# Performance work log

Measured on AMD Instinct MI355X. Metric: run time of the kernel, lower is better.

The kernel has to match this reference:

```python
import jax, jax.numpy as jnp
import numpy as np

B, S, D, DK = 8192, 3, 2048, 1024  # S fixed to 3 by Linear(3,3)/Bilinear(3,3,3)
NORM_FACT = 1.0 / np.sqrt(DK)


def setup_inputs() -> dict:
    key = jax.random.key(0)
    ks = jax.random.split(key, 9)
    s_lin = 1.0 / np.sqrt(D)
    s3 = 1.0 / np.sqrt(3.0)
    return {
        "img": jax.random.normal(ks[0], (B, S, D), jnp.float32),
        "text": jax.random.normal(ks[1], (B, S, D), jnp.float32),
        "Wq": jax.random.uniform(ks[2], (DK, D), jnp.float32, -s_lin, s_lin),
        "bq": jax.random.uniform(ks[3], (DK,), jnp.float32, -s_lin, s_lin),
        "Wk": jax.random.uniform(ks[4], (DK, D), jnp.float32, -s_lin, s_lin),
        "bk": jax.random.uniform(ks[5], (DK,), jnp.float32, -s_lin, s_lin),
        "Wj": jax.random.uniform(ks[6], (3, 3), jnp.float32, -s3, s3),
        "bj": jax.random.uniform(ks[7], (3,), jnp.float32, -s3, s3),
        "Wbil": jax.random.uniform(ks[8], (3, 3, 3), jnp.float32, -s3, s3),
    }


def reference(img, text, Wq, bq, Wk, bk, Wj, bj, Wbil):
    # Projections: [B, S, DK]
    Q_i = jnp.einsum("bsd,kd->bsk", img, Wq) + bq
    K_i = jnp.einsum("bsd,kd->bsk", img, Wk) + bk
    Q_t = jnp.einsum("bsd,kd->bsk", text, Wq) + bq
    K_t = jnp.einsum("bsd,kd->bsk", text, Wk) + bk

    # [B, S, S] attention maps; note: scale applied AFTER softmax (faithful to source)
    atten_it = jax.nn.softmax(jnp.einsum("bqk,bsk->bqs", Q_i, K_t), axis=-1) * NORM_FACT
    atten_ii = jax.nn.softmax(jnp.einsum("bqk,bsk->bqs", Q_i, K_i), axis=-1) * NORM_FACT
    atten_tt = jax.nn.softmax(jnp.einsum("bqk,bsk->bqs", Q_t, K_t), axis=-1) * NORM_FACT

    def j_lin(x):  # Linear(3,3) on last dim
        return jnp.einsum("bqs,os->bqo", x, Wj) + bj

    def bilinear(x1, x2):  # Bilinear(3,3,3, bias=False)
        return jnp.einsum("bqi,oij,bqj->bqo", x1, Wbil, x2)

    j_it = j_lin(atten_it)
    atten_i = bilinear(j_it, j_lin(atten_ii))
    atten_t = bilinear(j_it, j_lin(atten_tt))

    output_i = jnp.einsum("bqs,bsd->bqd", atten_i, img)
    output_t = jnp.einsum("bqs,bsd->bqd", atten_t, text)
    return (output_i, output_t)
```

## Files before the change

### kernel.cpp

```cpp
#include <hip/hip_runtime.h>

typedef unsigned short u16;
typedef unsigned int u32;
typedef __attribute__((ext_vector_type(8))) short short8;
typedef __attribute__((ext_vector_type(4))) float f32x4;

#define GLOBAL_AS __attribute__((address_space(1)))
#define LDS_AS __attribute__((address_space(3)))

__device__ __forceinline__ u16 f2bf(float f) {
  u32 u = __float_as_uint(f);
  u += 0x7fffu + ((u >> 16) & 1u);
  return (u16)(u >> 16);
}
__device__ __forceinline__ float bflo(u32 u) { return __uint_as_float(u << 16); }
__device__ __forceinline__ float bfhi(u32 u) { return __uint_as_float(u & 0xffff0000u); }

__device__ __forceinline__ void gload_lds16(const void* g, void* l) {
  __builtin_amdgcn_global_load_lds((const GLOBAL_AS void*)g, (LDS_AS void*)l, 16, 0, 0);
}

__global__ __launch_bounds__(256) void convert_all(
    const float4* __restrict__ img4, const float4* __restrict__ text4,
    const float4* __restrict__ wq4, const float4* __restrict__ wk4,
    const float4* __restrict__ bq4, const float4* __restrict__ bk4,
    ushort4* __restrict__ xbf4, ushort4* __restrict__ wcat4,
    float4* __restrict__ bcat4) {
  size_t id = (size_t)blockIdx.x * 256 + threadIdx.x;
  if (id < 25165824) {
    float4 v = (id < 12582912) ? img4[id] : text4[id - 12582912];
    ushort4 r; r.x = f2bf(v.x); r.y = f2bf(v.y); r.z = f2bf(v.z); r.w = f2bf(v.w);
    xbf4[id] = r;
  } else if (id < 26214400) {
    size_t j = id - 25165824;
    float4 v = (j < 524288) ? wq4[j] : wk4[j - 524288];
    ushort4 r; r.x = f2bf(v.x); r.y = f2bf(v.y); r.z = f2bf(v.z); r.w = f2bf(v.w);
    wcat4[j] = r;
  } else {
    size_t j = id - 26214400;
    bcat4[j] = (j < 256) ? bq4[j] : bk4[j - 256];
  }
}

__global__ __launch_bounds__(256) void gemm_qk(
    const u16* __restrict__ X, const u16* __restrict__ W,
    const float* __restrict__ bias, u16* __restrict__ QK) {
  __shared__ __align__(16) u16 As[128 * 32];
  __shared__ __align__(16) u16 Bs[128 * 32];
  const int t = threadIdx.x;
  const int lane = t & 63;
  const int wv = t >> 6;
  const int m0 = blockIdx.y * 128;
  const int n0 = blockIdx.x * 128;
  const int wm = (wv & 1) * 64;
  const int wn = (wv >> 1) * 64;
  const int fm = lane & 15;
  const int fq = lane >> 4;

  const int r0 = (wv * 2 + 0) * 16 + (lane >> 2);
  const int r1 = (wv * 2 + 1) * 16 + (lane >> 2);
  const int kc8 = (lane & 3) * 8;
  const u16* gA0 = X + (size_t)(m0 + r0) * 2048 + kc8;
  const u16* gA1 = X + (size_t)(m0 + r1) * 2048 + kc8;
  const u16* gB0 = W + (size_t)(n0 + r0) * 2048 + kc8;
  const u16* gB1 = W + (size_t)(n0 + r1) * 2048 + kc8;
  u16* lA0 = &As[(wv * 2 + 0) * 512];
  u16* lA1 = &As[(wv * 2 + 1) * 512];
  u16* lB0 = &Bs[(wv * 2 + 0) * 512];
  u16* lB1 = &Bs[(wv * 2 + 1) * 512];

  const f32x4 zero = {0.f, 0.f, 0.f, 0.f};
  f32x4 acc[4][4];
#pragma unroll
  for (int i = 0; i < 4; i++)
#pragma unroll
    for (int j = 0; j < 4; j++) acc[i][j] = zero;

  for (int kb = 0; kb < 2048; kb += 32) {
    __syncthreads();
    gload_lds16(gA0 + kb, lA0);
    gload_lds16(gA1 + kb, lA1);
    gload_lds16(gB0 + kb, lB0);
    gload_lds16(gB1 + kb, lB1);
    __syncthreads();

    short8 a[4], b[4];
#pragma unroll
    for (int i = 0; i < 4; i++) {
      a[i] = *(const short8*)&As[(wm + i * 16 + fm) * 32 + fq * 8];
      b[i] = *(const short8*)&Bs[(wn + i * 16 + fm) * 32 + fq * 8];
    }
#pragma unroll
    for (int i = 0; i < 4; i++)
#pragma unroll
      for (int j = 0; j < 4; j++)
        acc[i][j] = __builtin_amdgcn_mfma_f32_16x16x32_bf16(a[i], b[j], acc[i][j], 0, 0, 0);
  }

  float bn[4];
#pragma unroll
  for (int j = 0; j < 4; j++) bn[j] = bias[n0 + wn + j * 16 + fm];

#pragma unroll
  for (int i = 0; i < 4; i++) {
#pragma unroll
    for (int r = 0; r < 4; r++) {
      int mg = m0 + wm + i * 16 + fq * 4 + r;
      unsigned bb, idx, base;
      if (mg < 24576) { bb = (unsigned)mg / 3u; idx = (unsigned)mg - bb * 3u; base = 0u; }
      else { unsigned mt = (unsigned)mg - 24576u; bb = mt / 3u; idx = mt - bb * 3u; base = 6u; }
      size_t rowbase = (size_t)bb * 12288 + (size_t)(base + idx) * 1024;
#pragma unroll
      for (int j = 0; j < 4; j++) {
        int ng = n0 + wn + j * 16 + fm;
        size_t pos = rowbase + ((ng & 1024) ? 3072 : 0) + (ng & 1023);
        QK[pos] = f2bf(acc[i][j][r] + bn[j]);
      }
    }
  }
}

__global__ __launch_bounds__(256) void fuse_out(
    const float* __restrict__ img, const float* __restrict__ text,
    const float* __restrict__ Wj, const float* __restrict__ bjp,
    const float* __restrict__ Wb, float* __restrict__ out) {
  const int t = threadIdx.x;
  const int lane = t & 63;
  const int wv = t >> 6;
  const int b = blockIdx.x;

  const uint2* qkp = (const uint2*)((const char*)out + (size_t)b * 24576);

  float R[12][4];
#pragma unroll
  for (int r = 0; r < 12; r++) {
    uint2 u = qkp[r * 256 + t];
    R[r][0] = bflo(u.x); R[r][1] = bfhi(u.x);
    R[r][2] = bflo(u.y); R[r][3] = bfhi(u.y);
  }
  float acc[27];
#pragma unroll
  for (int a = 0; a < 27; a++) acc[a] = 0.f;
#pragma unroll
  for (int q = 0; q < 3; q++)
#pragma unroll
    for (int s = 0; s < 3; s++)
#pragma unroll
      for (int j = 0; j < 4; j++) {
        acc[q * 3 + s]      += R[q][j]     * R[9 + s][j];
        acc[9 + q * 3 + s]  += R[q][j]     * R[3 + s][j];
        acc[18 + q * 3 + s] += R[6 + q][j] * R[9 + s][j];
      }
#pragma unroll
  for (int a = 0; a < 27; a++) {
    float v = acc[a];
#pragma unroll
    for (int off = 32; off > 0; off >>= 1) v += __shfl_xor(v, off, 64);
    acc[a] = v;
  }
  __shared__ float red[4][27];
  if (lane == 0) {
#pragma unroll
    for (int a = 0; a < 27; a++) red[wv][a] = acc[a];
  }
  __syncthreads();
  float S[27];
#pragma unroll
  for (int a = 0; a < 27; a++) S[a] = red[0][a] + red[1][a] + red[2][a] + red[3][a];

  float P[27];
#pragma unroll
  for (int m = 0; m < 3; m++)
#pragma unroll
    for (int q = 0; q < 3; q++) {
      int o0 = m * 9 + q * 3;
      float x = S[o0], y = S[o0 + 1], z = S[o0 + 2];
      float mx = fmaxf(x, fmaxf(y, z));
      float e0 = __expf(x - mx), e1 = __expf(y - mx), e2 = __expf(z - mx);
      float inv = 0.03125f / (e0 + e1 + e2);
      P[o0] = e0 * inv; P[o0 + 1] = e1 * inv; P[o0 + 2] = e2 * inv;
    }
  float J[3][3][3];
#pragma unroll
  for (int m = 0; m < 3; m++)
#pragma unroll
    for (int q = 0; q < 3; q++)
#pragma unroll
      for (int o = 0; o < 3; o++)
        J[m][q][o] = bjp[o] + Wj[o * 3 + 0] * P[m * 9 + q * 3 + 0]
                            + Wj[o * 3 + 1] * P[m * 9 + q * 3 + 1]
                            + Wj[o * 3 + 2] * P[m * 9 + q * 3 + 2];
  float ai[3][3], at[3][3];
#pragma unroll
  for (int q = 0; q < 3; q++)
#pragma unroll
    for (int o = 0; o < 3; o++) {
      float s1 = 0.f, s2 = 0.f;
#pragma unroll
      for (int i = 0; i < 3; i++) {
        float a1 = J[0][q][i];
#pragma unroll
        for (int j = 0; j < 3; j++) {
          float w = Wb[(o * 3 + i) * 3 + j];
          s1 += a1 * w * J[1][q][j];
          s2 += a1 * w * J[2][q][j];
        }
      }
      ai[q][o] = s1; at[q][o] = s2;
    }

  const float4* im4 = (const float4*)(img + (size_t)b * 6144);
  const float4* tx4 = (const float4*)(text + (size_t)b * 6144);
  float4* oi4 = (float4*)out + (size_t)b * 1536;
  float4* ot4 = (float4*)out + 12582912 + (size_t)b * 1536;
#pragma unroll
  for (int rep = 0; rep < 2; rep++) {
    int col = rep * 256 + t;
    float4 x0 = im4[col], x1 = im4[512 + col], x2 = im4[1024 + col];
    float4 y0 = tx4[col], y1 = tx4[512 + col], y2 = tx4[1024 + col];
#pragma unroll
    for (int q = 0; q < 3; q++) {
      float4 o1, o2;
      o1.x = ai[q][0] * x0.x + ai[q][1] * x1.x + ai[q][2] * x2.x;
      o1.y = ai[q][0] * x0.y + ai[q][1] * x1.y + ai[q][2] * x2.y;
      o1.z = ai[q][0] * x0.z + ai[q][1] * x1.z + ai[q][2] * x2.z;
      o1.w = ai[q][0] * x0.w + ai[q][1] * x1.w + ai[q][2] * x2.w;
      oi4[q * 512 + col] = o1;
      o2.x = at[q][0] * y0.x + at[q][1] * y1.x + at[q][2] * y2.x;
      o2.y = at[q][0] * y0.y + at[q][1] * y1.y + at[q][2] * y2.y;
      o2.z = at[q][0] * y0.z + at[q][1] * y1.z + at[q][2] * y2.z;
      o2.w = at[q][0] * y0.w + at[q][1] * y1.w + at[q][2] * y2.w;
      ot4[q * 512 + col] = o2;
    }
  }
}

extern "C" void kernel_launch(void* const* d_in, const int* in_sizes, int n_in,
                              void* d_out, int out_size, void* d_ws, size_t ws_size,
                              hipStream_t stream) {
  const float* img  = (const float*)d_in[0];
  const float* text = (const float*)d_in[1];
  const float* Wq   = (const float*)d_in[2];
  const float* bq   = (const float*)d_in[3];
  const float* Wk   = (const float*)d_in[4];
  const float* bk   = (const float*)d_in[5];
  const float* Wj   = (const float*)d_in[6];
  const float* bj   = (const float*)d_in[7];
  const float* Wbil = (const float*)d_in[8];
  float* out = (float*)d_out;

  u16* Wcat = (u16*)d_ws;
  float* bcat = (float*)((char*)d_ws + 8388608);
  u16* Xbf = (u16*)(out + 50331648);
  u16* QK  = (u16*)out;

  convert_all<<<102402, 256, 0, stream>>>(
      (const float4*)img, (const float4*)text, (const float4*)Wq,
      (const float4*)Wk, (const float4*)bq, (const float4*)bk,
      (ushort4*)Xbf, (ushort4*)Wcat, (float4*)bcat);

  dim3 g(16, 384, 1);
  gemm_qk<<<g, 256, 0, stream>>>(Xbf, Wcat, bcat, QK);

  fuse_out<<<8192, 256, 0, stream>>>(img, text, Wj, bj, Wbil, out);
}
```

Before: 1.275 ms.

## Rewrite QK GEMM with 256x256 tiles, 4-stage LDS pipeline, and swizzling

The projection GEMM moves from 128x128 tiles with 4 waves and a fully synchronous load/compute loop to 256x256 tiles with 8 waves. A 4-deep global_load_lds ring buffer is kept in flight using vmcnt waits and a single barrier per k-step. LDS reads use XOR swizzling to reduce bank conflicts, block indices are remapped for L2 locality, and MFMA sections are wrapped in setprio. The intent is to hide memory latency and raise MFMA utilization. In exchange, the kernel needs 64KB of LDS per block, which may limit occupancy, and relies on hand-tuned waitcnt counts.

```diff
diff --git a/kernel.cpp b/kernel.cpp
--- a/kernel.cpp
+++ b/kernel.cpp
@@ -42,79 +42,120 @@
   }
 }
 
-__global__ __launch_bounds__(256) void gemm_qk(
+__global__ __launch_bounds__(512, 2) void gemm_qk(
     const u16* __restrict__ X, const u16* __restrict__ W,
     const float* __restrict__ bias, u16* __restrict__ QK) {
-  __shared__ __align__(16) u16 As[128 * 32];
-  __shared__ __align__(16) u16 Bs[128 * 32];
+  __shared__ __align__(16) u16 As[4][8192];
+  __shared__ __align__(16) u16 Bs[4][8192];
+
   const int t = threadIdx.x;
   const int lane = t & 63;
   const int wv = t >> 6;
-  const int m0 = blockIdx.y * 128;
-  const int n0 = blockIdx.x * 128;
-  const int wm = (wv & 1) * 64;
-  const int wn = (wv >> 1) * 64;
+  const int wm = wv >> 2;
+  const int wn = wv & 3;
   const int fm = lane & 15;
   const int fq = lane >> 4;
 
-  const int r0 = (wv * 2 + 0) * 16 + (lane >> 2);
-  const int r1 = (wv * 2 + 1) * 16 + (lane >> 2);
-  const int kc8 = (lane & 3) * 8;
-  const u16* gA0 = X + (size_t)(m0 + r0) * 2048 + kc8;
-  const u16* gA1 = X + (size_t)(m0 + r1) * 2048 + kc8;
-  const u16* gB0 = W + (size_t)(n0 + r0) * 2048 + kc8;
-  const u16* gB1 = W + (size_t)(n0 + r1) * 2048 + kc8;
-  u16* lA0 = &As[(wv * 2 + 0) * 512];
-  u16* lA1 = &As[(wv * 2 + 1) * 512];
-  u16* lB0 = &Bs[(wv * 2 + 0) * 512];
-  u16* lB1 = &Bs[(wv * 2 + 1) * 512];
+  const int swz = (blockIdx.x & 7) * 192 + (blockIdx.x >> 3);
+  const int m0 = (swz >> 3) * 256;
+  const int n0 = (swz & 7) * 256;
+
+  const int sr = lane >> 2;
+  const int sc = ((lane & 3) ^ ((lane >> 3) & 3)) * 8;
+  const u16* gA = X + (size_t)(m0 + wv * 32 + sr) * 2048 + sc;
+  const u16* gB = W + (size_t)(n0 + wv * 32 + sr) * 2048 + sc;
+  const int stgL = wv * 1024;
+
+  const int swz8 = (fq ^ ((fm >> 1) & 3)) * 8;
+  const int aOff = (wm * 128 + fm) * 32 + swz8;
+  const int bOff = (wn * 64 + fm) * 32 + swz8;
 
   const f32x4 zero = {0.f, 0.f, 0.f, 0.f};
-  f32x4 acc[4][4];
-#pragma unroll
-  for (int i = 0; i < 4; i++)
+  f32x4 acc[8][4];
+#pragma unroll
+  for (int i = 0; i < 8; i++)
 #pragma unroll
     for (int j = 0; j < 4; j++) acc[i][j] = zero;
 
-  for (int kb = 0; kb < 2048; kb += 32) {
-    __syncthreads();
-    gload_lds16(gA0 + kb, lA0);
-    gload_lds16(gA1 + kb, lA1);
-    gload_lds16(gB0 + kb, lB0);
-    gload_lds16(gB1 + kb, lB1);
-    __syncthreads();
-
+  auto STAGE = [&](int tile, int sb) {
+    const u16* ga = gA + (size_t)tile * 32;
+    const u16* gb = gB + (size_t)tile * 32;
+    u16* la = &As[sb][stgL];
+    u16* lb = &Bs[sb][stgL];
+    gload_lds16(ga, la);
+    gload_lds16(ga + 32768, la + 512);
+    gload_lds16(gb, lb);
+    gload_lds16(gb + 32768, lb + 512);
+  };
+
+  auto COMPUTE = [&](int buf) {
+    const u16* Ab = &As[buf][0];
+    const u16* Bb = &Bs[buf][0];
     short8 a[4], b[4];
 #pragma unroll
-    for (int i = 0; i < 4; i++) {
-      a[i] = *(const short8*)&As[(wm + i * 16 + fm) * 32 + fq * 8];
-      b[i] = *(const short8*)&Bs[(wn + i * 16 + fm) * 32 + fq * 8];
-    }
+    for (int j = 0; j < 4; j++) b[j] = *(const short8*)&Bb[bOff + j * 512];
+#pragma unroll
+    for (int i = 0; i < 4; i++) a[i] = *(const short8*)&Ab[aOff + i * 512];
+    __builtin_amdgcn_s_setprio(1);
 #pragma unroll
     for (int i = 0; i < 4; i++)
 #pragma unroll
       for (int j = 0; j < 4; j++)
         acc[i][j] = __builtin_amdgcn_mfma_f32_16x16x32_bf16(a[i], b[j], acc[i][j], 0, 0, 0);
-  }
+    __builtin_amdgcn_s_setprio(0);
+#pragma unroll
+    for (int i = 0; i < 4; i++) a[i] = *(const short8*)&Ab[aOff + 2048 + i * 512];
+    __builtin_amdgcn_s_setprio(1);
+#pragma unroll
+    for (int i = 0; i < 4; i++)
+#pragma unroll
+      for (int j = 0; j < 4; j++)
+        acc[4 + i][j] = __builtin_amdgcn_mfma_f32_16x16x32_bf16(a[i], b[j], acc[4 + i][j], 0, 0, 0);
+    __builtin_amdgcn_s_setprio(0);
+  };
+
+  STAGE(0, 0);
+  STAGE(1, 1);
+  STAGE(2, 2);
+
+  for (int kt = 0; kt < 61; ++kt) {
+    asm volatile("s_waitcnt vmcnt(8)" ::: "memory");
+    __builtin_amdgcn_s_barrier();
+    asm volatile("" ::: "memory");
+    STAGE(kt + 3, (kt + 3) & 3);
+    COMPUTE(kt & 3);
+  }
+  asm volatile("s_waitcnt vmcnt(8)" ::: "memory");
+  __builtin_amdgcn_s_barrier();
+  asm volatile("" ::: "memory");
+  COMPUTE(61 & 3);
+  asm volatile("s_waitcnt vmcnt(4)" ::: "memory");
+  __builtin_amdgcn_s_barrier();
+  asm volatile("" ::: "memory");
+  COMPUTE(62 & 3);
+  asm volatile("s_waitcnt vmcnt(0)" ::: "memory");
+  __builtin_amdgcn_s_barrier();
+  asm volatile("" ::: "memory");
+  COMPUTE(63 & 3);
 
   float bn[4];
 #pragma unroll
-  for (int j = 0; j < 4; j++) bn[j] = bias[n0 + wn + j * 16 + fm];
-
-#pragma unroll
-  for (int i = 0; i < 4; i++) {
+  for (int j = 0; j < 4; j++) bn[j] = bias[n0 + wn * 64 + j * 16 + fm];
+
+#pragma unroll
+  for (int mi = 0; mi < 8; mi++) {
 #pragma unroll
     for (int r = 0; r < 4; r++) {
-      int mg = m0 + wm + i * 16 + fq * 4 + r;
+      int mg = m0 + wm * 128 + mi * 16 + fq * 4 + r;
       unsigned bb, idx, base;
       if (mg < 24576) { bb = (unsigned)mg / 3u; idx = (unsigned)mg - bb * 3u; base = 0u; }
       else { unsigned mt = (unsigned)mg - 24576u; bb = mt / 3u; idx = mt - bb * 3u; base = 6u; }
       size_t rowbase = (size_t)bb * 12288 + (size_t)(base + idx) * 1024;
 #pragma unroll
       for (int j = 0; j < 4; j++) {
-        int ng = n0 + wn + j * 16 + fm;
+        int ng = n0 + wn * 64 + j * 16 + fm;
         size_t pos = rowbase + ((ng & 1024) ? 3072 : 0) + (ng & 1023);
-        QK[pos] = f2bf(acc[i][j][r] + bn[j]);
+        QK[pos] = f2bf(acc[mi][j][r] + bn[j]);
       }
     }
   }
@@ -259,8 +300,7 @@
       (const float4*)Wk, (const float4*)bq, (const float4*)bk,
       (ushort4*)Xbf, (ushort4*)Wcat, (float4*)bcat);
 
-  dim3 g(16, 384, 1);
-  gemm_qk<<<g, 256, 0, stream>>>(Xbf, Wcat, bcat, QK);
+  gemm_qk<<<1536, 512, 0, stream>>>(Xbf, Wcat, bcat, QK);
 
   fuse_out<<<8192, 256, 0, stream>>>(img, text, Wj, bj, Wbil, out);
 }
```

New measurement: 1.288 ms. No clear change (+1.0%).

## Rewrite QK GEMM as 256x256 double-buffered pipelined kernel with swizzled LDS

Applied to the files above, without the earlier changes.

Replaces the 128x128, K=32 single-buffered GEMM with a 256x256 tile, 512-thread, K=64 kernel. It double-buffers LDS and interleaves async global-to-LDS loads with MFMA phases under fine-grained barriers and s_setprio. It also XOR-swizzles LDS columns to avoid bank conflicts and remaps block indices for L2 locality. The aim is to hide memory latency and raise MFMA utilization, at the cost of heavy register and LDS use and a fragile hand-tuned waitcnt schedule.

```diff
diff --git a/kernel.cpp b/kernel.cpp
--- a/kernel.cpp
+++ b/kernel.cpp
@@ -42,82 +42,169 @@
   }
 }
 
-__global__ __launch_bounds__(256) void gemm_qk(
+__global__ __launch_bounds__(512, 2) void gemm_qk(
     const u16* __restrict__ X, const u16* __restrict__ W,
     const float* __restrict__ bias, u16* __restrict__ QK) {
-  __shared__ __align__(16) u16 As[128 * 32];
-  __shared__ __align__(16) u16 Bs[128 * 32];
+  __shared__ __align__(16) u16 Al[2][16384];
+  __shared__ __align__(16) u16 Bl[2][16384];
+
   const int t = threadIdx.x;
   const int lane = t & 63;
   const int wv = t >> 6;
-  const int m0 = blockIdx.y * 128;
-  const int n0 = blockIdx.x * 128;
-  const int wm = (wv & 1) * 64;
-  const int wn = (wv >> 1) * 64;
+  const int wm = wv >> 2;
+  const int wn = wv & 3;
   const int fm = lane & 15;
   const int fq = lane >> 4;
-
-  const int r0 = (wv * 2 + 0) * 16 + (lane >> 2);
-  const int r1 = (wv * 2 + 1) * 16 + (lane >> 2);
-  const int kc8 = (lane & 3) * 8;
-  const u16* gA0 = X + (size_t)(m0 + r0) * 2048 + kc8;
-  const u16* gA1 = X + (size_t)(m0 + r1) * 2048 + kc8;
-  const u16* gB0 = W + (size_t)(n0 + r0) * 2048 + kc8;
-  const u16* gB1 = W + (size_t)(n0 + r1) * 2048 + kc8;
-  u16* lA0 = &As[(wv * 2 + 0) * 512];
-  u16* lA1 = &As[(wv * 2 + 1) * 512];
-  u16* lB0 = &Bs[(wv * 2 + 0) * 512];
-  u16* lB1 = &Bs[(wv * 2 + 1) * 512];
+  const int l3 = lane >> 3;
+  const int l7 = lane & 7;
+
+  const int swz = (blockIdx.x & 7) * 192 + (blockIdx.x >> 3);
+  const int m0 = (swz >> 3) * 256;
+  const int n0 = (swz & 7) * 256;
+
+  const int kswz = (l7 ^ l3) * 8;
+  const int rA0 = wv * 8 + l3;
+  const int rB0 = (wv >> 2) * 64 + (wv & 3) * 8 + l3;
+  const u16* baseA = X + (size_t)(m0 + rA0) * 2048 + kswz;
+  const u16* baseB = W + (size_t)(n0 + rB0) * 2048 + kswz;
+
+  const int cx = fm & 7;
+  const int aRd = (wm * 128 + fm) * 64;
+  const int bRd = (wn * 64 + fm) * 64;
 
   const f32x4 zero = {0.f, 0.f, 0.f, 0.f};
-  f32x4 acc[4][4];
-#pragma unroll
-  for (int i = 0; i < 4; i++)
+  f32x4 acc[8][4];
+#pragma unroll
+  for (int i = 0; i < 8; i++)
 #pragma unroll
     for (int j = 0; j < 4; j++) acc[i][j] = zero;
 
-  for (int kb = 0; kb < 2048; kb += 32) {
-    __syncthreads();
-    gload_lds16(gA0 + kb, lA0);
-    gload_lds16(gA1 + kb, lA1);
-    gload_lds16(gB0 + kb, lB0);
-    gload_lds16(gB1 + kb, lB1);
-    __syncthreads();
-
-    short8 a[4], b[4];
-#pragma unroll
-    for (int i = 0; i < 4; i++) {
-      a[i] = *(const short8*)&As[(wm + i * 16 + fm) * 32 + fq * 8];
-      b[i] = *(const short8*)&Bs[(wn + i * 16 + fm) * 32 + fq * 8];
-    }
-#pragma unroll
-    for (int i = 0; i < 4; i++)
-#pragma unroll
-      for (int j = 0; j < 4; j++)
-        acc[i][j] = __builtin_amdgcn_mfma_f32_16x16x32_bf16(a[i], b[j], acc[i][j], 0, 0, 0);
+  short8 a[4][2], bl[2][2], bh[2][2];
+
+#define STAGE_A(buf, half, tt) do {                                        \
+    const u16* s_ = baseA + (size_t)(tt) * 64 + (half) * 131072;           \
+    u16* d_ = &Al[buf][wv * 512 + (half) * 4096];                          \
+    gload_lds16(s_, d_);                                                   \
+    gload_lds16(s_ + 262144, d_ + 8192);                                   \
+  } while (0)
+#define STAGE_B(buf, half, tt) do {                                        \
+    const u16* s_ = baseB + (size_t)(tt) * 64 + (half) * 65536;            \
+    u16* d_ = &Bl[buf][(wv >> 2) * 4096 + (wv & 3) * 512 + (half) * 2048]; \
+    gload_lds16(s_, d_);                                                   \
+    gload_lds16(s_ + 262144, d_ + 8192);                                   \
+  } while (0)
+
+#define RD_A(buf, h) do {                                                  \
+    _Pragma("unroll") for (int mi = 0; mi < 4; mi++)                       \
+    _Pragma("unroll") for (int kk = 0; kk < 2; kk++)                       \
+      a[mi][kk] = *(const short8*)&Al[buf][aRd + (h) * 4096 + mi * 1024 +  \
+                                           ((((kk << 2) | fq) ^ cx) * 8)]; \
+  } while (0)
+#define RD_B(buf, h, bb) do {                                              \
+    _Pragma("unroll") for (int nj = 0; nj < 2; nj++)                       \
+    _Pragma("unroll") for (int kk = 0; kk < 2; kk++)                       \
+      bb[nj][kk] = *(const short8*)&Bl[buf][bRd + (h) * 2048 + nj * 1024 + \
+                                            ((((kk << 2) | fq) ^ cx) * 8)];\
+  } while (0)
+
+#define MM(R, Cb, bb) do {                                                 \
+    __builtin_amdgcn_s_setprio(1);                                         \
+    _Pragma("unroll") for (int mi = 0; mi < 4; mi++)                       \
+    _Pragma("unroll") for (int nj = 0; nj < 2; nj++)                       \
+    _Pragma("unroll") for (int kk = 0; kk < 2; kk++)                       \
+      acc[(R) + mi][(Cb) + nj] = __builtin_amdgcn_mfma_f32_16x16x32_bf16(  \
+          a[mi][kk], bb[nj][kk], acc[(R) + mi][(Cb) + nj], 0, 0, 0);       \
+    __builtin_amdgcn_s_setprio(0);                                         \
+  } while (0)
+
+#define BAR1_LGKM() do {                                                   \
+    asm volatile("" ::: "memory");                                         \
+    __builtin_amdgcn_s_barrier();                                          \
+    asm volatile("s_waitcnt lgkmcnt(0)" ::: "memory");                     \
+    __builtin_amdgcn_sched_barrier(0);                                     \
+  } while (0)
+#define BAR2(N) do {                                                       \
+    asm volatile("s_waitcnt vmcnt(" #N ")" ::: "memory");                  \
+    __builtin_amdgcn_s_barrier();                                          \
+    asm volatile("" ::: "memory");                                         \
+  } while (0)
+
+  STAGE_A(0, 0, 0);
+  STAGE_B(0, 0, 0);
+  STAGE_B(0, 1, 0);
+  STAGE_A(0, 1, 0);
+  asm volatile("s_waitcnt vmcnt(4)" ::: "memory");
+  __builtin_amdgcn_s_barrier();
+  asm volatile("" ::: "memory");
+
+  for (int kt = 0; kt < 31; ++kt) {
+    const int c = kt & 1, o = c ^ 1;
+    RD_A(c, 0);
+    RD_B(c, 0, bl);
+    STAGE_A(o, 0, kt + 1);
+    BAR1_LGKM();
+    MM(0, 0, bl);
+    BAR2(4);
+    RD_B(c, 1, bh);
+    STAGE_B(o, 0, kt + 1);
+    BAR1_LGKM();
+    MM(0, 2, bh);
+    BAR2(4);
+    RD_A(c, 1);
+    STAGE_B(o, 1, kt + 1);
+    BAR1_LGKM();
+    MM(4, 0, bl);
+    BAR2(4);
+    STAGE_A(o, 1, kt + 1);
+    BAR1_LGKM();
+    MM(4, 2, bh);
+    BAR2(4);
+  }
+
+  {
+    RD_A(1, 0);
+    RD_B(1, 0, bl);
+    BAR1_LGKM();
+    MM(0, 0, bl);
+    BAR2(2);
+    RD_B(1, 1, bh);
+    BAR1_LGKM();
+    MM(0, 2, bh);
+    BAR2(0);
+    RD_A(1, 1);
+    BAR1_LGKM();
+    MM(4, 0, bl);
+    MM(4, 2, bh);
   }
 
   float bn[4];
 #pragma unroll
-  for (int j = 0; j < 4; j++) bn[j] = bias[n0 + wn + j * 16 + fm];
-
-#pragma unroll
-  for (int i = 0; i < 4; i++) {
+  for (int j = 0; j < 4; j++) bn[j] = bias[n0 + wn * 64 + j * 16 + fm];
+
+#pragma unroll
+  for (int mi = 0; mi < 8; mi++) {
 #pragma unroll
     for (int r = 0; r < 4; r++) {
-      int mg = m0 + wm + i * 16 + fq * 4 + r;
+      int mg = m0 + wm * 128 + mi * 16 + fq * 4 + r;
       unsigned bb, idx, base;
       if (mg < 24576) { bb = (unsigned)mg / 3u; idx = (unsigned)mg - bb * 3u; base = 0u; }
       else { unsigned mt = (unsigned)mg - 24576u; bb = mt / 3u; idx = mt - bb * 3u; base = 6u; }
       size_t rowbase = (size_t)bb * 12288 + (size_t)(base + idx) * 1024;
 #pragma unroll
       for (int j = 0; j < 4; j++) {
-        int ng = n0 + wn + j * 16 + fm;
+        int ng = n0 + wn * 64 + j * 16 + fm;
         size_t pos = rowbase + ((ng & 1024) ? 3072 : 0) + (ng & 1023);
-        QK[pos] = f2bf(acc[i][j][r] + bn[j]);
+        QK[pos] = f2bf(acc[mi][j][r] + bn[j]);
       }
     }
   }
+#undef STAGE_A
+#undef STAGE_B
+#undef RD_A
+#undef RD_B
+#undef MM
+#undef BAR1_LGKM
+#undef BAR2
 }
 
 __global__ __launch_bounds__(256) void fuse_out(
@@ -259,8 +346,7 @@
       (const float4*)Wk, (const float4*)bq, (const float4*)bk,
       (ushort4*)Xbf, (ushort4*)Wcat, (float4*)bcat);
 
-  dim3 g(16, 384, 1);
-  gemm_qk<<<g, 256, 0, stream>>>(Xbf, Wcat, bcat, QK);
+  gemm_qk<<<1536, 512, 0, stream>>>(Xbf, Wcat, bcat, QK);
 
   fuse_out<<<8192, 256, 0, stream>>>(img, text, Wj, bj, Wbil, out);
 }
```

Result: faster. 1.224 ms (-4.0%).
